# Kernel tuning notes

Hardware: AMD Instinct MI355X
Metric: run time of the kernel (lower is better)

The kernel has to match this reference:

```python
import jax, jax.numpy as jnp
import numpy as np

B, N, T = 8, 512, 24
HID, HOR, NID, NBLOCKS, NHIDL = 256, 24, 64, 3, 2  # block_layers=3 -> 1 input layer + 2 hidden
D = T + N * T + NID  # FcBlock input size = 12376


def div_no_nan(a, b):
    safe = jnp.where(b == 0, jnp.ones_like(b), b)
    return jnp.where(b == 0, jnp.zeros_like(a), a / safe)


def setup_inputs() -> dict:
    key = jax.random.key(0)
    ks = jax.random.split(key, 16)
    s_in = 1.0 / np.sqrt(D)
    s_h = 1.0 / np.sqrt(HID)
    return {
        "history_in": jax.random.uniform(ks[0], (B, N, T), jnp.float32),
        "node_id_in": jax.random.randint(ks[1], (B, N, 1), 0, N, dtype=jnp.int32),
        "time_of_day_in": jax.random.uniform(ks[2], (B, N, 1), jnp.float32),
        "adjacency_in": jax.random.uniform(ks[3], (B, N, N), jnp.float32),
        "node_emb": jax.random.uniform(ks[4], (N, NID), jnp.float32, -0.05, 0.05),
        "W_in": jax.random.normal(ks[5], (NBLOCKS, D, HID), jnp.float32) * s_in,
        "b_in": jnp.zeros((NBLOCKS, HID), jnp.float32),
        "W_hid": jax.random.normal(ks[6], (NBLOCKS, NHIDL, HID, HID), jnp.float32) * s_h,
        "b_hid": jnp.zeros((NBLOCKS, NHIDL, HID), jnp.float32),
        "W_f": jax.random.normal(ks[7], (NBLOCKS, HID, HOR), jnp.float32) * s_h,
        "b_f": jnp.zeros((NBLOCKS, HOR), jnp.float32),
        "W_b": jax.random.normal(ks[8], (NBLOCKS, HID, D), jnp.float32) * s_h,
        "b_b": jnp.zeros((NBLOCKS, D), jnp.float32),
    }


def fc_block(x, W_in, b_in, W_hid, b_hid, W_f, b_f, W_b, b_b):
    # x: [B, N, D]
    h = jax.nn.relu(jnp.einsum('bnd,dh->bnh', x, W_in) + b_in)
    for l in range(NHIDL):
        h = jax.nn.relu(jnp.einsum('bnh,hk->bnk', h, W_hid[l]) + b_hid[l])
    forecast = jnp.einsum('bnh,ho->bno', h, W_f) + b_f
    backcast = jax.nn.relu(x - (jnp.einsum('bnh,hd->bnd', h, W_b) + b_b))
    return backcast, forecast


def reference(history_in, node_id_in, time_of_day_in, adjacency_in, node_emb,
              W_in, b_in, W_hid, b_hid, W_f, b_f, W_b, b_b):
    # node id embedding: [B,N,1] -> [B,N,1,NID] -> squeeze -> [B,N,NID]
    node_id = node_emb[node_id_in[..., 0]]

    # use_time_gate=False: time_gate_forward = 0, time_gate_backward = 0
    # history_in = history_in / (1 + 0) -> unchanged

    # graph_layer_type == 'none' branch with graph_adj = adjacency_in [B,N,N]
    level = jnp.max(history_in, axis=-1, keepdims=True)          # [B,N,1]
    history = div_no_nan(history_in, level)                      # [B,N,T]

    # tile history to all pairs and weight by adjacency: [B,N,N,T]
    all_node_history = adjacency_in[..., None] * history_in[:, None, :, :]
    all_node_history = all_node_history.reshape(B, N, N * T)     # [B,N,N*T]
    all_node_history = div_no_nan(all_node_history - level, level)
    all_node_history = jnp.where(all_node_history > 0, all_node_history, 0.0)

    history = jnp.concatenate([history, all_node_history, node_id], axis=-1)  # [B,N,D]

    backcast, forecast_out = fc_block(history, W_in[0], b_in[0], W_hid[0], b_hid[0],
                                      W_f[0], b_f[0], W_b[0], b_b[0])
    for i in range(1, NBLOCKS):
        backcast, fb = fc_block(backcast, W_in[i], b_in[i], W_hid[i], b_hid[i],
                                W_f[i], b_f[i], W_b[i], b_b[i])
        forecast_out = forecast_out + fb

    forecast_out = forecast_out[:, :, :HOR]
    forecast = forecast_out * level  # (1 + time_gate_forward) = 1
    return backcast, forecast
```

## Files before the change

kernel.cpp:

```cpp
#include <hip/hip_runtime.h>

#define Bq   8
#define Nn   512
#define Tt   24
#define NIDc 64
#define HIDc 256
#define HORc 24
#define Dd   12376
#define Mm   4096
#define DdPad 12384
#define NbPad 12416
#define SPLITK 8
#define KCHUNK 1568

typedef float  f32x4  __attribute__((ext_vector_type(4)));
typedef short  bf16x8 __attribute__((ext_vector_type(8)));

__device__ __forceinline__ ushort f2bf(float f) {
    unsigned u = __float_as_uint(f);
    u += 0x7FFF + ((u >> 16) & 1);
    return (ushort)(u >> 16);
}
__device__ __forceinline__ float bf2f(ushort h) {
    return __uint_as_float(((unsigned)h) << 16);
}

#define ASYNC16(g, l) __builtin_amdgcn_global_load_lds(                        \
    (const __attribute__((address_space(1))) unsigned*)(g),                    \
    (__attribute__((address_space(3))) unsigned*)(l), 16, 0, 0)

__global__ __launch_bounds__(256) void build_x_kernel(
    const float* __restrict__ hist, const int* __restrict__ nid,
    const float* __restrict__ adj, const float* __restrict__ emb,
    ushort* __restrict__ x, float* __restrict__ level)
{
    int bn = blockIdx.x;
    int b  = bn >> 9;
    __shared__ float sh[Tt];
    __shared__ float slv;
    int tid = threadIdx.x;
    const float* hrow = hist + (size_t)bn * Tt;
    if (tid < Tt) sh[tid] = hrow[tid];
    __syncthreads();
    if (tid == 0) {
        float m = sh[0];
        #pragma unroll
        for (int t = 1; t < Tt; t++) m = fmaxf(m, sh[t]);
        slv = m;
        level[bn] = m;
    }
    __syncthreads();
    float lv  = slv;
    float inv = (lv == 0.0f) ? 0.0f : 1.0f / lv;
    ushort* xr = x + (size_t)bn * DdPad;
    if (tid < Tt) xr[tid] = f2bf(sh[tid] * inv);
    const float* hb   = hist + (size_t)b * Nn * Tt;
    const float* arow = adj  + (size_t)bn * Nn;
    for (int base = tid * 8; base < Nn * Tt; base += 256 * 8) {
        bf16x8 pack;
        #pragma unroll
        for (int e = 0; e < 8; e++) {
            int idx = base + e;
            int m_ = idx / Tt;
            int t  = idx - m_ * Tt;
            float v = arow[m_] * hb[m_ * Tt + t];
            float r = (v - lv) * inv;
            pack[e] = (short)f2bf((r > 0.0f) ? r : 0.0f);
        }
        *(bf16x8*)(xr + Tt + base) = pack;
    }
    if (tid < NIDc) {
        int id = nid[bn];
        xr[Tt + Nn * Tt + tid] = f2bf(emb[(size_t)id * NIDc + tid]);
    }
    if (tid < DdPad - Dd) xr[Dd + tid] = 0;
}

__global__ __launch_bounds__(256) void transpose_w(
    const float* __restrict__ W0, ushort* __restrict__ Bt0,
    int K, int N, int Kpad, size_t wstep, size_t btstep)
{
    const float*  W  = W0  + (size_t)blockIdx.z * wstep;
    ushort*       Bt = Bt0 + (size_t)blockIdx.z * btstep;
    __shared__ ushort tile[32][72];
    const int k0 = blockIdx.x * 32;
    const int n0 = blockIdx.y * 64;
    const int tid = threadIdx.x;
    #pragma unroll
    for (int i = 0; i < 8; i++) {
        const int idx = tid + i * 256;
        const int kk = idx >> 6;
        const int nn = idx & 63;
        const int gk = k0 + kk, gn = n0 + nn;
        const float v = (gk < K && gn < N) ? W[(size_t)gk * N + gn] : 0.0f;
        tile[kk][nn] = f2bf(v);
    }
    __syncthreads();
    const int n  = tid >> 2;
    const int kc = (tid & 3) << 3;
    uint4 o;
    o.x = (unsigned)tile[kc + 0][n] | ((unsigned)tile[kc + 1][n] << 16);
    o.y = (unsigned)tile[kc + 2][n] | ((unsigned)tile[kc + 3][n] << 16);
    o.z = (unsigned)tile[kc + 4][n] | ((unsigned)tile[kc + 5][n] << 16);
    o.w = (unsigned)tile[kc + 6][n] | ((unsigned)tile[kc + 7][n] << 16);
    *(uint4*)(Bt + (size_t)(n0 + n) * Kpad + k0 + kc) = o;
}

template <int TM, int TN, int EPI>
__global__ __launch_bounds__(256) void gemm_mfma(
    const ushort* __restrict__ A, int lda,
    const ushort* __restrict__ Bt, int ldbt,
    const float* __restrict__ bias,
    const ushort* __restrict__ X, int ldx,
    void* __restrict__ Cp, int ldc,
    int K, int N, int chunk)
{
    constexpr int WI = TM / 32;
    constexpr int WJ = TN / 32;
    constexpr int SA = TM / 16;
    constexpr int SB = TN / 16;
    constexpr int LPW = (SA + SB) / 4;
    static_assert((SA + SB) % 4 == 0, "uniform loads per wave required");
    static_assert(LPW == 1 || LPW == 2 || LPW == 4, "vmcnt literal");
    __shared__ ushort As[2][TM * 32];
    __shared__ ushort Bs[2][TN * 32];

    const int tid  = threadIdx.x;
    const int row0 = blockIdx.x * TM;
    const int col0 = blockIdx.y * TN;
    const int spl  = blockIdx.z;
    const int kstart = spl * chunk;
    const int kend   = min(K, kstart + chunk);
    const int iters  = (kend - kstart) >> 5;

    const int lane = tid & 63;
    const int wave = tid >> 6;
    const int quad = lane >> 4;
    const int l15  = lane & 15;
    const int wm   = (wave >> 1) * (TM / 2);
    const int wn   = (wave & 1) * (TN / 2);

    f32x4 acc[WI][WJ];
    #pragma unroll
    for (int i = 0; i < WI; i++)
        #pragma unroll
        for (int j = 0; j < WJ; j++)
            acc[i][j] = (f32x4){0.f, 0.f, 0.f, 0.f};

    auto stage = [&](int buf, int kb) {
        #pragma unroll
        for (int t = 0; t < LPW; t++) {
            const int s = wave + 4 * t;
            if (s < SA) {
                const int r = s * 16 + (lane >> 2);
                ASYNC16(A + (size_t)(row0 + r) * lda + kb + ((lane & 3) << 3),
                        &As[buf][s * 512]);
            } else {
                const int s2 = s - SA;
                const int r = s2 * 16 + (lane >> 2);
                ASYNC16(Bt + (size_t)(col0 + r) * ldbt + kb + ((lane & 3) << 3),
                        &Bs[buf][s2 * 512]);
            }
        }
    };

    stage(0, kstart);

    float4  bpre[WJ];
    ushort4 xpre[WI][WJ];
    bool    cok[WJ];
    #pragma unroll
    for (int j = 0; j < WJ; j++) {
        const int c0 = col0 + wn + j * 16 + quad * 4;
        cok[j] = (c0 < N);
        if constexpr (EPI >= 2) {
            bpre[j] = cok[j] ? *(const float4*)&bias[c0]
                             : float4{0.f, 0.f, 0.f, 0.f};
        }
    }
    if constexpr (EPI >= 2) {
        #pragma unroll
        for (int i = 0; i < WI; i++) {
            const int row = row0 + wm + i * 16 + l15;
            #pragma unroll
            for (int j = 0; j < WJ; j++) {
                const int c0 = col0 + wn + j * 16 + quad * 4;
                xpre[i][j] = cok[j]
                    ? *(const ushort4*)&X[(size_t)row * ldx + c0]
                    : ushort4{0, 0, 0, 0};
            }
        }
    }

    for (int kt = 0; kt < iters; ++kt) {
        const int cur = kt & 1;
        if (kt + 1 < iters) {
            stage(cur ^ 1, kstart + ((kt + 1) << 5));
            if constexpr (LPW == 4)
                asm volatile("s_waitcnt vmcnt(4)" ::: "memory");
            else if constexpr (LPW == 2)
                asm volatile("s_waitcnt vmcnt(2)" ::: "memory");
            else
                asm volatile("s_waitcnt vmcnt(1)" ::: "memory");
        } else {
            asm volatile("s_waitcnt vmcnt(0)" ::: "memory");
        }
        __builtin_amdgcn_s_barrier();
        __builtin_amdgcn_sched_barrier(0);

        bf16x8 af[WI], bfr[WJ];
        #pragma unroll
        for (int i = 0; i < WI; i++)
            af[i] = *(const bf16x8*)&As[cur][(wm + i * 16 + l15) * 32 + quad * 8];
        #pragma unroll
        for (int j = 0; j < WJ; j++)
            bfr[j] = *(const bf16x8*)&Bs[cur][(wn + j * 16 + l15) * 32 + quad * 8];
        #pragma unroll
        for (int i = 0; i < WI; i++)
            #pragma unroll
            for (int j = 0; j < WJ; j++)
                acc[i][j] = __builtin_amdgcn_mfma_f32_16x16x32_bf16(
                    bfr[j], af[i], acc[i][j], 0, 0, 0);

        __builtin_amdgcn_sched_barrier(0);
        __builtin_amdgcn_s_barrier();
    }

    #pragma unroll
    for (int i = 0; i < WI; i++) {
        const int row = row0 + wm + i * 16 + l15;
        #pragma unroll
        for (int j = 0; j < WJ; j++) {
            const int c0 = col0 + wn + j * 16 + quad * 4;
            const f32x4 v = acc[i][j];
            if constexpr (EPI == 0) {
                *(f32x4*)&((float*)Cp)[(size_t)spl * Mm * HIDc +
                                       (size_t)row * ldc + c0] = v;
            } else if constexpr (EPI == 2) {
                if (cok[j]) {
                    f32x4 o;
                    o[0] = fmaxf(bf2f(xpre[i][j].x) - (v[0] + bpre[j].x), 0.f);
                    o[1] = fmaxf(bf2f(xpre[i][j].y) - (v[1] + bpre[j].y), 0.f);
                    o[2] = fmaxf(bf2f(xpre[i][j].z) - (v[2] + bpre[j].z), 0.f);
                    o[3] = fmaxf(bf2f(xpre[i][j].w) - (v[3] + bpre[j].w), 0.f);
                    *(f32x4*)&((float*)Cp)[(size_t)row * ldc + c0] = o;
                }
            } else {
                if (cok[j]) {
                    ushort4 o;
                    o.x = f2bf(fmaxf(bf2f(xpre[i][j].x) - (v[0] + bpre[j].x), 0.f));
                    o.y = f2bf(fmaxf(bf2f(xpre[i][j].y) - (v[1] + bpre[j].y), 0.f));
                    o.z = f2bf(fmaxf(bf2f(xpre[i][j].z) - (v[2] + bpre[j].z), 0.f));
                    o.w = f2bf(fmaxf(bf2f(xpre[i][j].w) - (v[3] + bpre[j].w), 0.f));
                    *(ushort4*)&((ushort*)Cp)[(size_t)row * ldc + c0] = o;
                }
            }
        }
    }
}

__global__ __launch_bounds__(256) void gemm_hidden(
    const ushort* __restrict__ A,
    const ushort* __restrict__ Bt,
    const float* __restrict__ bias,
    ushort* __restrict__ C)
{
    __shared__ ushort As[32 * 512];
    __shared__ ushort Bs[32 * 512];

    const int tid  = threadIdx.x;
    const int row0 = blockIdx.x * 64;
    const int col0 = blockIdx.y * 64;
    const int lane = tid & 63;
    const int wave = tid >> 6;
    const int quad = lane >> 4;
    const int l15  = lane & 15;
    const int wm   = (wave >> 1) * 32;
    const int wn   = (wave & 1) * 32;

    #pragma unroll
    for (int t = 0; t < 8; t++) {
        const int s = wave + 4 * t;
        const int kt = s >> 2;
        const int r  = ((s & 3) << 4) + (lane >> 2);
        ASYNC16(A + (size_t)(row0 + r) * HIDc + (kt << 5) + ((lane & 3) << 3),
                &As[s * 512]);
    }
    #pragma unroll
    for (int t = 0; t < 8; t++) {
        const int s = wave + 4 * t;
        const int kt = s >> 2;
        const int r  = ((s & 3) << 4) + (lane >> 2);
        ASYNC16(Bt + (size_t)(col0 + r) * HIDc + (kt << 5) + ((lane & 3) << 3),
                &Bs[s * 512]);
    }

    float4 bpre[2];
    #pragma unroll
    for (int j = 0; j < 2; j++)
        bpre[j] = *(const float4*)&bias[col0 + wn + j * 16 + quad * 4];

    f32x4 acc[2][2];
    #pragma unroll
    for (int i = 0; i < 2; i++)
        #pragma unroll
        for (int j = 0; j < 2; j++)
            acc[i][j] = (f32x4){0.f, 0.f, 0.f, 0.f};

    asm volatile("s_waitcnt vmcnt(0)" ::: "memory");
    __builtin_amdgcn_s_barrier();
    __builtin_amdgcn_sched_barrier(0);

    #pragma unroll
    for (int kt = 0; kt < 8; kt++) {
        bf16x8 af[2], bfr[2];
        #pragma unroll
        for (int i = 0; i < 2; i++) {
            const int r = wm + i * 16 + l15;
            af[i] = *(const bf16x8*)&As[(kt * 4 + (r >> 4)) * 512 +
                                        (r & 15) * 32 + quad * 8];
        }
        #pragma unroll
        for (int j = 0; j < 2; j++) {
            const int r = wn + j * 16 + l15;
            bfr[j] = *(const bf16x8*)&Bs[(kt * 4 + (r >> 4)) * 512 +
                                         (r & 15) * 32 + quad * 8];
        }
        #pragma unroll
        for (int i = 0; i < 2; i++)
            #pragma unroll
            for (int j = 0; j < 2; j++)
                acc[i][j] = __builtin_amdgcn_mfma_f32_16x16x32_bf16(
                    bfr[j], af[i], acc[i][j], 0, 0, 0);
    }

    #pragma unroll
    for (int i = 0; i < 2; i++) {
        const int row = row0 + wm + i * 16 + l15;
        #pragma unroll
        for (int j = 0; j < 2; j++) {
            const int c0 = col0 + wn + j * 16 + quad * 4;
            const f32x4 v = acc[i][j];
            ushort4 o;
            o.x = f2bf(fmaxf(v[0] + bpre[j].x, 0.f));
            o.y = f2bf(fmaxf(v[1] + bpre[j].y, 0.f));
            o.z = f2bf(fmaxf(v[2] + bpre[j].z, 0.f));
            o.w = f2bf(fmaxf(v[3] + bpre[j].w, 0.f));
            *(ushort4*)&C[(size_t)row * HIDc + c0] = o;
        }
    }
}

__global__ __launch_bounds__(256) void reduce_hin(
    const float* __restrict__ partial, const float* __restrict__ bias,
    ushort* __restrict__ h)
{
    const int gid = (blockIdx.x * 256 + threadIdx.x) * 4;
    f32x4 s = *(const f32x4*)&bias[gid & (HIDc - 1)];
    #pragma unroll
    for (int j = 0; j < SPLITK; j++)
        s += *(const f32x4*)&partial[(size_t)j * (Mm * HIDc) + gid];
    ushort4 o;
    o.x = f2bf(fmaxf(s[0], 0.f));
    o.y = f2bf(fmaxf(s[1], 0.f));
    o.z = f2bf(fmaxf(s[2], 0.f));
    o.w = f2bf(fmaxf(s[3], 0.f));
    *(ushort4*)&h[gid] = o;
}

__global__ __launch_bounds__(256) void gemm_forecast_kernel(
    const ushort* __restrict__ h, const float* __restrict__ Wf,
    const float* __restrict__ bf, float* __restrict__ fc,
    const float* __restrict__ level, float* __restrict__ out, int accumulate)
{
    int gid = blockIdx.x * 256 + threadIdx.x;
    if (gid >= Mm * HORc) return;
    int row = gid / HORc;
    int col = gid - row * HORc;
    const ushort* hr = h + (size_t)row * HIDc;
    float acc = 0.0f;
    #pragma unroll 4
    for (int k = 0; k < HIDc; k++)
        acc = fmaf(bf2f(hr[k]), Wf[k * HORc + col], acc);
    acc += bf[col];
    if (accumulate) acc += fc[gid];
    if (level) out[gid] = acc * level[row];
    else       fc[gid]  = acc;
}

extern "C" void kernel_launch(void* const* d_in, const int* in_sizes, int n_in,
                              void* d_out, int out_size, void* d_ws, size_t ws_size,
                              hipStream_t stream)
{
    const float* hist  = (const float*)d_in[0];
    const int*   nid   = (const int*)  d_in[1];
    const float* adj   = (const float*)d_in[3];
    const float* emb   = (const float*)d_in[4];
    const float* W_in  = (const float*)d_in[5];
    const float* b_in  = (const float*)d_in[6];
    const float* W_hid = (const float*)d_in[7];
    const float* b_hid = (const float*)d_in[8];
    const float* W_f   = (const float*)d_in[9];
    const float* b_f   = (const float*)d_in[10];
    const float* W_b   = (const float*)d_in[11];
    const float* b_b   = (const float*)d_in[12];

    float* bout = (float*)d_out;
    float* fout = (float*)d_out + (size_t)Mm * Dd;

    char* ws = (char*)d_ws;
    size_t off = 0;
    float*  level = (float*) (ws + off); off += 16384;
    float*  fc    = (float*) (ws + off); off += (size_t)Mm * HORc * 4;
    ushort* hA    = (ushort*)(ws + off); off += (size_t)Mm * HIDc * 2;
    ushort* hB    = (ushort*)(ws + off); off += (size_t)Mm * HIDc * 2;
    ushort* WtIn  = (ushort*)(ws + off); off += (size_t)3 * HIDc * DdPad * 2;
    ushort* WtHid = (ushort*)(ws + off); off += (size_t)6 * HIDc * HIDc * 2;
    ushort* WtB   = (ushort*)(ws + off); off += (size_t)3 * NbPad * HIDc * 2;
    float*  part  = (float*) (ws + off); off += (size_t)SPLITK * Mm * HIDc * 4;
    ushort* xb    = (ushort*)(ws + off); off += (size_t)Mm * DdPad * 2;

    build_x_kernel<<<Mm, 256, 0, stream>>>(hist, nid, adj, emb, xb, level);

    transpose_w<<<dim3(DdPad / 32, HIDc / 64, 3), 256, 0, stream>>>(
        W_in, WtIn, Dd, HIDc, DdPad,
        (size_t)Dd * HIDc, (size_t)HIDc * DdPad);
    transpose_w<<<dim3(HIDc / 32, HIDc / 64, 6), 256, 0, stream>>>(
        W_hid, WtHid, HIDc, HIDc, HIDc,
        (size_t)HIDc * HIDc, (size_t)HIDc * HIDc);
    transpose_w<<<dim3(HIDc / 32, NbPad / 64, 3), 256, 0, stream>>>(
        W_b, WtB, HIDc, Dd, HIDc,
        (size_t)HIDc * Dd, (size_t)NbPad * HIDc);

    for (int i = 0; i < 3; i++) {
        const float* bi  = b_in  + (size_t)i * HIDc;
        const float* bh0 = b_hid + (size_t)(i * 2 + 0) * HIDc;
        const float* bh1 = b_hid + (size_t)(i * 2 + 1) * HIDc;
        const float* Wfi = W_f   + (size_t)i * HIDc * HORc;
        const float* bfi = b_f   + (size_t)i * HORc;
        const float* bbi = b_b   + (size_t)i * Dd;

        gemm_mfma<128, 128, 0>
            <<<dim3(Mm / 128, HIDc / 128, SPLITK), 256, 0, stream>>>(
            xb, DdPad, WtIn + (size_t)i * HIDc * DdPad, DdPad,
            nullptr, nullptr, 0, part, HIDc, DdPad, HIDc, KCHUNK);
        reduce_hin<<<Mm * HIDc / 1024, 256, 0, stream>>>(part, bi, hA);

        gemm_hidden<<<dim3(Mm / 64, HIDc / 64), 256, 0, stream>>>(
            hA, WtHid + (size_t)(2 * i) * HIDc * HIDc, bh0, hB);
        gemm_hidden<<<dim3(Mm / 64, HIDc / 64), 256, 0, stream>>>(
            hB, WtHid + (size_t)(2 * i + 1) * HIDc * HIDc, bh1, hA);

        gemm_forecast_kernel<<<(Mm * HORc + 255) / 256, 256, 0, stream>>>(
            hA, Wfi, bfi, fc, (i == 2) ? level : nullptr, fout, i > 0 ? 1 : 0);

        if (i < 2) {
            gemm_mfma<128, 128, 3>
                <<<dim3(Mm / 128, NbPad / 128, 1), 256, 0, stream>>>(
                hA, HIDc, WtB + (size_t)i * NbPad * HIDc, HIDc,
                bbi, xb, DdPad, xb, DdPad, HIDc, Dd, HIDc);
        } else {
            gemm_mfma<128, 128, 2>
                <<<dim3(Mm / 128, NbPad / 128, 1), 256, 0, stream>>>(
                hA, HIDc, WtB + (size_t)i * NbPad * HIDc, HIDc,
                bbi, xb, DdPad, bout, Dd, HIDc, Dd, HIDc);
        }
    }
}
```

Before: 856.2 us.

## Triple-buffer GEMM shared tiles and swizzle backcast GEMM block order

The MFMA GEMM moves from double to triple buffering in shared memory. It prefetches two K-tiles ahead, with the vmcnt waits adjusted to match, so more global-load latency is hidden. The backcast GEMMs now launch on a 1D grid with an XCD-aware swizzle that maps consecutive blocks to the same column tile, which should improve L2 reuse of weight tiles across the chiplets. The cost is 50% more LDS per block, which may lower occupancy, and the swizzle is hard-coded to 32 row blocks and 8 XCDs.

```diff
diff --git a/kernel.cpp b/kernel.cpp
--- a/kernel.cpp
+++ b/kernel.cpp
@@ -106,7 +106,7 @@
     *(uint4*)(Bt + (size_t)(n0 + n) * Kpad + k0 + kc) = o;
 }
 
-template <int TM, int TN, int EPI>
+template <int TM, int TN, int EPI, int SWZ>
 __global__ __launch_bounds__(256) void gemm_mfma(
     const ushort* __restrict__ A, int lda,
     const ushort* __restrict__ Bt, int ldbt,
@@ -122,13 +122,23 @@
     constexpr int LPW = (SA + SB) / 4;
     static_assert((SA + SB) % 4 == 0, "uniform loads per wave required");
     static_assert(LPW == 1 || LPW == 2 || LPW == 4, "vmcnt literal");
-    __shared__ ushort As[2][TM * 32];
-    __shared__ ushort Bs[2][TN * 32];
+    __shared__ ushort As[3][TM * 32];
+    __shared__ ushort Bs[3][TN * 32];
 
     const int tid  = threadIdx.x;
-    const int row0 = blockIdx.x * TM;
-    const int col0 = blockIdx.y * TN;
-    const int spl  = blockIdx.z;
+    int row0, col0, spl;
+    if constexpr (SWZ) {
+        static_assert(TM == 128, "swizzle assumes Mm/TM == 32 row-blocks");
+        const int cpx = (int)gridDim.x >> 3;
+        const int swz = ((int)blockIdx.x & 7) * cpx + ((int)blockIdx.x >> 3);
+        row0 = (swz & 31) * TM;
+        col0 = (swz >> 5) * TN;
+        spl  = 0;
+    } else {
+        row0 = blockIdx.x * TM;
+        col0 = blockIdx.y * TN;
+        spl  = blockIdx.z;
+    }
     const int kstart = spl * chunk;
     const int kend   = min(K, kstart + chunk);
     const int iters  = (kend - kstart) >> 5;
@@ -165,6 +175,7 @@
     };
 
     stage(0, kstart);
+    if (iters > 1) stage(1, kstart + 32);
 
     float4  bpre[WJ];
     ushort4 xpre[WI][WJ];
@@ -192,10 +203,18 @@
         }
     }
 
+    int cur = 0;
     for (int kt = 0; kt < iters; ++kt) {
-        const int cur = kt & 1;
-        if (kt + 1 < iters) {
-            stage(cur ^ 1, kstart + ((kt + 1) << 5));
+        if (kt + 2 < iters) {
+            int b2 = cur + 2; if (b2 >= 3) b2 -= 3;
+            stage(b2, kstart + ((kt + 2) << 5));
+            if constexpr (LPW == 4)
+                asm volatile("s_waitcnt vmcnt(8)" ::: "memory");
+            else if constexpr (LPW == 2)
+                asm volatile("s_waitcnt vmcnt(4)" ::: "memory");
+            else
+                asm volatile("s_waitcnt vmcnt(2)" ::: "memory");
+        } else if (kt + 1 < iters) {
             if constexpr (LPW == 4)
                 asm volatile("s_waitcnt vmcnt(4)" ::: "memory");
             else if constexpr (LPW == 2)
@@ -224,6 +243,7 @@
 
         __builtin_amdgcn_sched_barrier(0);
         __builtin_amdgcn_s_barrier();
+        cur = (cur == 2) ? 0 : cur + 1;
     }
 
     #pragma unroll
@@ -440,7 +460,7 @@
         const float* bfi = b_f   + (size_t)i * HORc;
         const float* bbi = b_b   + (size_t)i * Dd;
 
-        gemm_mfma<128, 128, 0>
+        gemm_mfma<128, 128, 0, 0>
             <<<dim3(Mm / 128, HIDc / 128, SPLITK), 256, 0, stream>>>(
             xb, DdPad, WtIn + (size_t)i * HIDc * DdPad, DdPad,
             nullptr, nullptr, 0, part, HIDc, DdPad, HIDc, KCHUNK);
@@ -455,13 +475,13 @@
             hA, Wfi, bfi, fc, (i == 2) ? level : nullptr, fout, i > 0 ? 1 : 0);
 
         if (i < 2) {
-            gemm_mfma<128, 128, 3>
-                <<<dim3(Mm / 128, NbPad / 128, 1), 256, 0, stream>>>(
+            gemm_mfma<128, 128, 3, 1>
+                <<<dim3((Mm / 128) * (NbPad / 128)), 256, 0, stream>>>(
                 hA, HIDc, WtB + (size_t)i * NbPad * HIDc, HIDc,
                 bbi, xb, DdPad, xb, DdPad, HIDc, Dd, HIDc);
         } else {
-            gemm_mfma<128, 128, 2>
-                <<<dim3(Mm / 128, NbPad / 128, 1), 256, 0, stream>>>(
+            gemm_mfma<128, 128, 2, 1>
+                <<<dim3((Mm / 128) * (NbPad / 128)), 256, 0, stream>>>(
                 hA, HIDc, WtB + (size_t)i * NbPad * HIDc, HIDc,
                 bbi, xb, DdPad, bout, Dd, HIDc, Dd, HIDc);
         }
```

New measurement: 889.0 us. +3.8%, slower.
